# Performance work log

Measured on AMD Instinct MI355X. Metric: run time of the kernel, lower is better.

The kernel has to match this reference:

```python
import jax, jax.numpy as jnp
import numpy as np

C = 384; H = 32; W = 32; HEADS = 12; HD = C // HEADS; MLP = 1536
KOFF = 5; OFF_RANGE = 2.0


def layer_norm(x, g, b, eps=1e-5):
    mu = jnp.mean(x, axis=-1, keepdims=True)
    var = jnp.mean(jnp.square(x - mu), axis=-1, keepdims=True)
    return (x - mu) * jax.lax.rsqrt(var + eps) * g + b


def depthwise_conv(x, k):
    # x: (B,H,W,C), k: (kh,kw,1,C), SAME padding, groups=C
    return jax.lax.conv_general_dilated(
        x, k, window_strides=(1, 1), padding='SAME',
        dimension_numbers=('NHWC', 'HWIO', 'NHWC'), feature_group_count=C)


def grid_sample_bilinear(img, pos):
    # img: (B,H,W,C); pos: (B,H,W,2) normalized (y,x) in [-1,1], align_corners=True, border clamp
    B, Hh, Ww, Cc = img.shape
    py = (pos[..., 0] + 1.0) * 0.5 * (Hh - 1)
    px = (pos[..., 1] + 1.0) * 0.5 * (Ww - 1)
    y0 = jnp.floor(py); x0 = jnp.floor(px)
    wy = (py - y0)[..., None]; wx = (px - x0)[..., None]
    y0i = jnp.clip(y0.astype(jnp.int32), 0, Hh - 1)
    y1i = jnp.clip(y0i + 1, 0, Hh - 1)
    x0i = jnp.clip(x0.astype(jnp.int32), 0, Ww - 1)
    x1i = jnp.clip(x0i + 1, 0, Ww - 1)
    b = jnp.arange(B)[:, None, None]
    g = lambda yi, xi: img[b, yi, xi]
    return (g(y0i, x0i) * (1 - wy) * (1 - wx) + g(y0i, x1i) * (1 - wy) * wx
            + g(y1i, x0i) * wy * (1 - wx) + g(y1i, x1i) * wy * wx)


def setup_inputs() -> dict:
    key = jax.random.key(0)
    ks = jax.random.split(key, 16)
    n = jax.random.normal
    s = 0.02
    inp = {
        'x': n(ks[0], (16, H * W, C), jnp.float32),
        'ln1_g': jnp.ones((C,), jnp.float32), 'ln1_b': jnp.zeros((C,), jnp.float32),
        'Wq': n(ks[1], (C, C), jnp.float32) * s, 'bq': jnp.zeros((C,), jnp.float32),
        'off_k': n(ks[2], (KOFF, KOFF, 1, C), jnp.float32) * s,
        'off_kb': jnp.zeros((C,), jnp.float32),
        'offln_g': jnp.ones((C,), jnp.float32), 'offln_b': jnp.zeros((C,), jnp.float32),
        'Woff': n(ks[3], (2, C), jnp.float32) * s, 'boff': jnp.zeros((2,), jnp.float32),
        'Wk': n(ks[4], (C, C), jnp.float32) * s, 'bk': jnp.zeros((C,), jnp.float32),
        'Wv': n(ks[5], (C, C), jnp.float32) * s, 'bv': jnp.zeros((C,), jnp.float32),
        'Wo': n(ks[6], (C, C), jnp.float32) * s, 'bo': jnp.zeros((C,), jnp.float32),
        'ln2_g': jnp.ones((C,), jnp.float32), 'ln2_b': jnp.zeros((C,), jnp.float32),
        'W1': n(ks[7], (MLP, C), jnp.float32) * s, 'b1': jnp.zeros((MLP,), jnp.float32),
        'W2': n(ks[8], (C, MLP), jnp.float32) * s, 'b2': jnp.zeros((C,), jnp.float32),
    }
    return inp


def _block(x, ln1_g, ln1_b, Wq, bq, off_k, off_kb, offln_g, offln_b, Woff, boff,
           Wk, bk, Wv, bv, Wo, bo, ln2_g, ln2_b, W1, b1, W2, b2):
    B, N, _ = x.shape
    # --- deformable attention branch ---
    xn = layer_norm(x, ln1_g, ln1_b)
    xi = xn.reshape(B, H, W, C)
    q = xi @ Wq.T + bq                                  # (B,H,W,C)
    # offset network: depthwise conv -> LN -> GELU -> 1x1 conv to 2
    off = depthwise_conv(q, off_k) + off_kb
    off = jax.nn.gelu(layer_norm(off, offln_g, offln_b))
    off = off @ Woff.T + boff                           # (B,H,W,2)
    off_range = jnp.array([OFF_RANGE * 2.0 / H, OFF_RANGE * 2.0 / W], jnp.float32)
    off = jnp.tanh(off) * off_range                     # normalized coord units
    ry = (jnp.arange(H, dtype=jnp.float32) + 0.5) / H * 2.0 - 1.0
    rx = (jnp.arange(W, dtype=jnp.float32) + 0.5) / W * 2.0 - 1.0
    ref = jnp.stack(jnp.meshgrid(ry, rx, indexing='ij'), axis=-1)  # (H,W,2)
    pos = ref[None] + off                               # (B,H,W,2)
    xs = grid_sample_bilinear(xi, pos).reshape(B, N, C)  # sampled keys/values source
    k = xs @ Wk.T + bk
    v = xs @ Wv.T + bv
    qh = q.reshape(B, N, HEADS, HD).transpose(0, 2, 1, 3)
    kh = k.reshape(B, N, HEADS, HD).transpose(0, 2, 1, 3)
    vh = v.reshape(B, N, HEADS, HD).transpose(0, 2, 1, 3)
    attn = jax.nn.softmax(jnp.einsum('bhqd,bhkd->bhqk', qh, kh) * (HD ** -0.5), axis=-1)
    o = jnp.einsum('bhqk,bhkd->bhqd', attn, vh).transpose(0, 2, 1, 3).reshape(B, N, C)
    x = x + (o @ Wo.T + bo)
    # --- MLP branch ---
    y = layer_norm(x, ln2_g, ln2_b)
    y = jax.nn.gelu(y @ W1.T + b1) @ W2.T + b2
    return x + y


def reference(x, ln1_g, ln1_b, Wq, bq, off_k, off_kb, offln_g, offln_b, Woff, boff,
              Wk, bk, Wv, bv, Wo, bo, ln2_g, ln2_b, W1, b1, W2, b2):
    return _block(x, ln1_g, ln1_b, Wq, bq, off_k, off_kb, offln_g, offln_b, Woff, boff,
                  Wk, bk, Wv, bv, Wo, bo, ln2_g, ln2_b, W1, b1, W2, b2)
```

## Files before the change

### kernel.cpp

```cpp
#include <hip/hip_runtime.h>
#include <math.h>

#define DI __device__ __forceinline__

typedef __attribute__((ext_vector_type(8))) short bf16x8;
typedef __attribute__((ext_vector_type(4))) float f32x4;

static constexpr int CC = 384;
static constexpr float QSCALE = 0.17677669529663687f * 1.4426950408889634f;
static constexpr float INVQS  = 1.0f / QSCALE;

DI unsigned short f2bf(float f){
  unsigned u = __float_as_uint(f);
  u += 0x7FFFu + ((u >> 16) & 1u);
  return (unsigned short)(u >> 16);
}
DI float bf2f(unsigned short u){ return __uint_as_float((unsigned)u << 16); }
DI float lo16(unsigned u){ return __uint_as_float(u << 16); }
DI float hi16(unsigned u){ return __uint_as_float(u & 0xFFFF0000u); }
DI float fexp2(float x){ return __builtin_amdgcn_exp2f(x); }
DI float frcp(float x){ return __builtin_amdgcn_rcpf(x); }
DI float tanh_fast(float z){ return 1.f - 2.f*frcp(fexp2(2.8853900817779268f*z) + 1.f); }
DI float gelu_fast(float v){
  float u = v*v;
  float z = 0.7978845608028654f * fmaf(0.044715f*u, v, v);
  return v - v*frcp(fexp2(2.8853900817779268f*z) + 1.f);
}
DI f32x4 mfma16(bf16x8 a, bf16x8 b, f32x4 c){
  return __builtin_amdgcn_mfma_f32_16x16x32_bf16(a, b, c, 0, 0, 0);
}
DI void gload16(const unsigned short* g, unsigned short* l){
  __builtin_amdgcn_global_load_lds(
      (const __attribute__((address_space(1))) unsigned int*)(const void*)g,
      (__attribute__((address_space(3))) unsigned int*)(void*)l, 16, 0, 0);
}
DI unsigned packbf(float pa, float pb){
  return __builtin_amdgcn_perm(__float_as_uint(pb), __float_as_uint(pa), 0x07060302u);
}

__global__ __launch_bounds__(256) void k_cvt_all(
    const float* __restrict__ wq, const float* __restrict__ wk,
    const float* __restrict__ wv, const float* __restrict__ wo,
    const float* __restrict__ w1, const float* __restrict__ w2,
    const float* __restrict__ ofk,
    unsigned short* __restrict__ dst)
{
  int i4 = (blockIdx.x*256 + threadIdx.x)*4;
  if (i4 >= 1779072) return;
  const float* src; int off;
  if (i4 < 147456){ src = wq; off = i4; }
  else if (i4 < 294912){ src = wk; off = i4 - 147456; }
  else if (i4 < 442368){ src = wv; off = i4 - 294912; }
  else if (i4 < 589824){ src = wo; off = i4 - 442368; }
  else if (i4 < 1179648){ src = w1; off = i4 - 589824; }
  else if (i4 < 1769472){ src = w2; off = i4 - 1179648; }
  else { src = ofk; off = i4 - 1769472; }
  float4 v = *(const float4*)(src + off);
  uint2 o;
  o.x = ((unsigned)f2bf(v.y) << 16) | f2bf(v.x);
  o.y = ((unsigned)f2bf(v.w) << 16) | f2bf(v.z);
  *(uint2*)(dst + i4) = o;
}

template<int BIN>
__global__ __launch_bounds__(256) void k_ln(const float* __restrict__ xf,
    const unsigned short* __restrict__ xb,
    const float* __restrict__ g, const float* __restrict__ b,
    unsigned short* __restrict__ outb)
{
  int row = blockIdx.x*4 + (threadIdx.x >> 6);
  int l = threadIdx.x & 63;
  float v[6]; int ch[6];
  if constexpr (BIN){
    int cA = 4*l, cB = 256 + 2*l;
    ch[0]=cA; ch[1]=cA+1; ch[2]=cA+2; ch[3]=cA+3; ch[4]=cB; ch[5]=cB+1;
    const unsigned short* xp = xb + (size_t)row * CC;
    uint2 u2 = *(const uint2*)(xp + cA);
    unsigned u1 = *(const unsigned*)(xp + cB);
    v[0]=lo16(u2.x); v[1]=hi16(u2.x); v[2]=lo16(u2.y); v[3]=hi16(u2.y);
    v[4]=lo16(u1);   v[5]=hi16(u1);
  } else {
    const float* xp = xf + (size_t)row * CC;
#pragma unroll
    for (int p = 0; p < 6; p++){ ch[p] = l + 64*p; v[p] = xp[ch[p]]; }
  }
  float s = 0.f, s2 = 0.f;
#pragma unroll
  for (int p = 0; p < 6; p++){ s += v[p]; s2 += v[p]*v[p]; }
#pragma unroll
  for (int m = 32; m; m >>= 1){ s += __shfl_xor(s, m); s2 += __shfl_xor(s2, m); }
  float mu = s * (1.f/CC);
  float var = s2 * (1.f/CC) - mu*mu;
  float rs = rsqrtf(var + 1e-5f);
  float o[6];
#pragma unroll
  for (int p = 0; p < 6; p++) o[p] = (v[p] - mu) * rs * g[ch[p]] + b[ch[p]];
  unsigned short* op = outb + (size_t)row*CC;
  if constexpr (BIN){
    uint2 st;
    st.x = ((unsigned)f2bf(o[1]) << 16) | f2bf(o[0]);
    st.y = ((unsigned)f2bf(o[3]) << 16) | f2bf(o[2]);
    *(uint2*)(op + ch[0]) = st;
    *(unsigned*)(op + ch[4]) = ((unsigned)f2bf(o[5]) << 16) | f2bf(o[4]);
  } else {
#pragma unroll
    for (int p = 0; p < 6; p++) op[ch[p]] = f2bf(o[p]);
  }
}

template<int EPI>
__global__ __launch_bounds__(256) void k_gemm64(
    const unsigned short* __restrict__ A, const unsigned short* __restrict__ W,
    const float* __restrict__ bias, const float* __restrict__ bias2,
    const float* __restrict__ res, const unsigned short* __restrict__ resb,
    float* __restrict__ outf, unsigned short* __restrict__ outb,
    unsigned short* __restrict__ outb2, int ntn, int N, int K)
{
  __shared__ unsigned short As[2][2048];
  __shared__ unsigned short Bs[2][4096];
  int bid = blockIdx.x;
  int cpx = gridDim.x >> 3;
  int id = (bid & 7)*cpx + (bid >> 3);
  int bn = (id % ntn) * 128;
  int bm = (id / ntn) * 64;
  int t = threadIdx.x;
  int w = t >> 6, l = t & 63;
  int g = l >> 4, ln = l & 15;
  int wm = w >> 1, wn = w & 1;
  f32x4 acc[2][4];
#pragma unroll
  for (int i = 0; i < 2; i++)
#pragma unroll
    for (int j = 0; j < 4; j++) acc[i][j] = (f32x4){0.f,0.f,0.f,0.f};
  int srow = t >> 2, slot = t & 3;
  int srowB = srow + 64;
  int cb0 = (slot ^ (srow  & 3) ^ ((srow  >> 2) & 3)) * 8;
  int cb1 = (slot ^ (srowB & 3) ^ ((srowB >> 2) & 3)) * 8;
  const unsigned short* Ap  = A + (size_t)(bm + srow)*K + cb0;
  const unsigned short* Wp0 = W + (size_t)(bn + srow)*K + cb0;
  const unsigned short* Wp1 = W + (size_t)(bn + srowB)*K + cb1;
  int NT = K >> 5;
  int wl = w*512;
  gload16(Ap,  &As[0][wl]);
  gload16(Wp0, &Bs[0][wl]);
  gload16(Wp1, &Bs[0][wl + 2048]);
  __syncthreads();
  for (int kt = 0; kt < NT; kt++){
    int cur = kt & 1;
    if (kt + 1 < NT){
      int k0 = (kt + 1) << 5;
      gload16(Ap  + k0, &As[cur ^ 1][wl]);
      gload16(Wp0 + k0, &Bs[cur ^ 1][wl]);
      gload16(Wp1 + k0, &Bs[cur ^ 1][wl + 2048]);
    }
    bf16x8 af[2], bf[4];
#pragma unroll
    for (int mi = 0; mi < 2; mi++){
      int row = wm*32 + mi*16 + ln;
      int sl = g ^ (row & 3) ^ ((row >> 2) & 3);
      af[mi] = *(const bf16x8*)((const char*)As[cur] + row*64 + sl*16);
    }
#pragma unroll
    for (int ni = 0; ni < 4; ni++){
      int row = wn*64 + ni*16 + ln;
      int sl = g ^ (row & 3) ^ ((row >> 2) & 3);
      bf[ni] = *(const bf16x8*)((const char*)Bs[cur] + row*64 + sl*16);
    }
#pragma unroll
    for (int mi = 0; mi < 2; mi++)
#pragma unroll
      for (int ni = 0; ni < 4; ni++)
        acc[mi][ni] = mfma16(af[mi], bf[ni], acc[mi][ni]);
    if (kt + 1 < NT) __syncthreads();
  }
#pragma unroll
  for (int mi = 0; mi < 2; mi++)
#pragma unroll
  for (int ni = 0; ni < 4; ni++){
    int col = bn + wn*64 + ni*16 + ln;
    float bv;
    if constexpr (EPI == 6) bv = col < 384 ? bias[col] : bias2[col - 384];
    else bv = bias[col];
#pragma unroll
    for (int i = 0; i < 4; i++){
      int row = bm + wm*32 + mi*16 + g*4 + i;
      float v = acc[mi][ni][i] + bv;
      if constexpr (EPI == 2){ v += res[(size_t)row*N + col]; outb[(size_t)row*N + col] = f2bf(v); }
      if constexpr (EPI == 7){ v += bf2f(resb[(size_t)row*N + col]); outf[(size_t)row*N + col] = v; }
      if constexpr (EPI == 3) v = gelu_fast(v);
      if constexpr (EPI == 0) outf[(size_t)row*N + col] = v;
      if constexpr (EPI == 1 || EPI == 3) outb[(size_t)row*N + col] = f2bf(v);
      if constexpr (EPI == 5) outb[(size_t)row*N + col] = f2bf(v * QSCALE);
      if constexpr (EPI == 6){
        if (col < 384){
          outb[(size_t)row*384 + col] = f2bf(v);
        } else {
          int c = col - 384;
          int bb = row >> 10, key = row & 1023, h = c >> 5, d = c & 31;
          int k6 = key & 63;
          int phys = (key & ~63) | (k6 & 0x23) | ((k6 & 0xC) << 1) | ((k6 & 0x10) >> 2);
          outb2[(size_t)(((bb*12 + h) << 5) + d)*1024 + phys] = f2bf(v);
        }
      }
    }
  }
}

__global__ __launch_bounds__(256) void k_mlp1(
    const unsigned short* __restrict__ A, const unsigned short* __restrict__ W,
    const float* __restrict__ bias, unsigned short* __restrict__ outb)
{
  __shared__ unsigned short As[2][4096];
  __shared__ unsigned short Bs[2][4096];
  int bid = blockIdx.x;
  int cpx = gridDim.x >> 3;
  int id = (bid & 7)*cpx + (bid >> 3);
  int bn = (id % 12) * 128;
  int bm = (id / 12) * 128;
  int t = threadIdx.x;
  int w = t >> 6, l = t & 63;
  int g = l >> 4, ln = l & 15;
  int wm = w >> 1, wn = w & 1;
  f32x4 acc[4][4];
#pragma unroll
  for (int i = 0; i < 4; i++)
#pragma unroll
    for (int j = 0; j < 4; j++) acc[i][j] = (f32x4){0.f,0.f,0.f,0.f};
  int srow0 = t >> 2, slot = t & 3;
  int srow1 = srow0 + 64;
  int cb0 = (slot ^ (srow0 & 3) ^ ((srow0 >> 2) & 3)) * 8;
  int cb1 = (slot ^ (srow1 & 3) ^ ((srow1 >> 2) & 3)) * 8;
  const unsigned short* Ap0 = A + (size_t)(bm + srow0)*384 + cb0;
  const unsigned short* Ap1 = A + (size_t)(bm + srow1)*384 + cb1;
  const unsigned short* Wp0 = W + (size_t)(bn + srow0)*384 + cb0;
  const unsigned short* Wp1 = W + (size_t)(bn + srow1)*384 + cb1;
  int wl = w*512;
  gload16(Ap0, &As[0][wl]);
  gload16(Ap1, &As[0][wl + 2048]);
  gload16(Wp0, &Bs[0][wl]);
  gload16(Wp1, &Bs[0][wl + 2048]);
  __syncthreads();
  for (int kt = 0; kt < 12; kt++){
    int cur = kt & 1;
    if (kt < 11){
      int k0 = (kt + 1) << 5;
      gload16(Ap0 + k0, &As[cur ^ 1][wl]);
      gload16(Ap1 + k0, &As[cur ^ 1][wl + 2048]);
      gload16(Wp0 + k0, &Bs[cur ^ 1][wl]);
      gload16(Wp1 + k0, &Bs[cur ^ 1][wl + 2048]);
    }
    bf16x8 af[4], bf[4];
#pragma unroll
    for (int mi = 0; mi < 4; mi++){
      int row = wm*64 + mi*16 + ln;
      int sl = g ^ (row & 3) ^ ((row >> 2) & 3);
      af[mi] = *(const bf16x8*)((const char*)As[cur] + row*64 + sl*16);
    }
#pragma unroll
    for (int ni = 0; ni < 4; ni++){
      int row = wn*64 + ni*16 + ln;
      int sl = g ^ (row & 3) ^ ((row >> 2) & 3);
      bf[ni] = *(const bf16x8*)((const char*)Bs[cur] + row*64 + sl*16);
    }
#pragma unroll
    for (int mi = 0; mi < 4; mi++)
#pragma unroll
      for (int ni = 0; ni < 4; ni++)
        acc[mi][ni] = mfma16(af[mi], bf[ni], acc[mi][ni]);
    if (kt < 11) __syncthreads();
  }
#pragma unroll
  for (int mi = 0; mi < 4; mi++)
#pragma unroll
  for (int ni = 0; ni < 4; ni++){
    int col = bn + wn*64 + ni*16 + ln;
    float bv = bias[col];
#pragma unroll
    for (int i = 0; i < 4; i++){
      int row = bm + wm*64 + mi*16 + g*4 + i;
      float v = gelu_fast(acc[mi][ni][i] + bv);
      outb[(size_t)row*1536 + col] = f2bf(v);
    }
  }
}

__global__ __launch_bounds__(64) void k_offset_sample(
    const unsigned short* __restrict__ qs, const unsigned short* __restrict__ xnb,
    const unsigned short* __restrict__ okb,
    const float* __restrict__ offkb,
    const float* __restrict__ offg, const float* __restrict__ offb,
    const float* __restrict__ Woff, const float* __restrict__ boff,
    unsigned short* __restrict__ xsb)
{
  int blk = blockIdx.x;
  int pix = (blk & 7)*2048 + (blk >> 3);
  int b = pix >> 10, n = pix & 1023;
  int y = n >> 5, x = n & 31;
  int t = threadIdx.x;
  int c8 = (t < 48 ? t : 47) * 8;
  float act = t < 48 ? 1.f : 0.f;
  const unsigned short* qb = qs + (size_t)b*1024*CC;
  int ry[5], rx[5]; unsigned my[5], mx[5];
#pragma unroll
  for (int k = 0; k < 5; k++){
    int yy = y + k - 2, xx = x + k - 2;
    my[k] = (yy >= 0 && yy < 32) ? 0xFFFFFFFFu : 0u;
    mx[k] = (xx >= 0 && xx < 32) ? 0xFFFFFFFFu : 0u;
    int yc = yy < 0 ? 0 : (yy > 31 ? 31 : yy);
    int xc = xx < 0 ? 0 : (xx > 31 ? 31 : xx);
    ry[k] = yc*32*CC; rx[k] = xc*CC;
  }
  float a[8];
#pragma unroll
  for (int j = 0; j < 8; j++) a[j] = 0.f;
#pragma unroll
  for (int ky = 0; ky < 5; ky++)
#pragma unroll
  for (int kx = 0; kx < 5; kx++){
    int tap = ky*5 + kx;
    unsigned m = my[ky] & mx[kx];
    uint4 q4 = *(const uint4*)(qb + ry[ky] + rx[kx] + c8);
    uint4 w4 = *(const uint4*)(okb + tap*CC + c8);
    q4.x &= m; q4.y &= m; q4.z &= m; q4.w &= m;
    a[0] = fmaf(lo16(q4.x), lo16(w4.x), a[0]);
    a[1] = fmaf(hi16(q4.x), hi16(w4.x), a[1]);
    a[2] = fmaf(lo16(q4.y), lo16(w4.y), a[2]);
    a[3] = fmaf(hi16(q4.y), hi16(w4.y), a[3]);
    a[4] = fmaf(lo16(q4.z), lo16(w4.z), a[4]);
    a[5] = fmaf(hi16(q4.z), hi16(w4.z), a[5]);
    a[6] = fmaf(lo16(q4.w), lo16(w4.w), a[6]);
    a[7] = fmaf(hi16(q4.w), hi16(w4.w), a[7]);
  }
  float4 kbA = *(const float4*)(offkb + c8);
  float4 kbB = *(const float4*)(offkb + c8 + 4);
  float c[8];
  c[0] = act * fmaf(a[0], INVQS, kbA.x);
  c[1] = act * fmaf(a[1], INVQS, kbA.y);
  c[2] = act * fmaf(a[2], INVQS, kbA.z);
  c[3] = act * fmaf(a[3], INVQS, kbA.w);
  c[4] = act * fmaf(a[4], INVQS, kbB.x);
  c[5] = act * fmaf(a[5], INVQS, kbB.y);
  c[6] = act * fmaf(a[6], INVQS, kbB.z);
  c[7] = act * fmaf(a[7], INVQS, kbB.w);
  float s = 0.f, s2 = 0.f;
#pragma unroll
  for (int j = 0; j < 8; j++){ s += c[j]; s2 += c[j]*c[j]; }
#pragma unroll
  for (int m2 = 32; m2; m2 >>= 1){ s += __shfl_xor(s, m2); s2 += __shfl_xor(s2, m2); }
  float mu = s * (1.f/CC);
  float var = s2 * (1.f/CC) - mu*mu;
  float rs = rsqrtf(var + 1e-5f);
  float4 gA = *(const float4*)(offg + c8); float4 gB = *(const float4*)(offg + c8 + 4);
  float4 oA = *(const float4*)(offb + c8); float4 oB = *(const float4*)(offb + c8 + 4);
  float4 wA = *(const float4*)(Woff + c8); float4 wB = *(const float4*)(Woff + c8 + 4);
  float4 wC = *(const float4*)(Woff + CC + c8); float4 wD = *(const float4*)(Woff + CC + c8 + 4);
  float gg[8] = {gA.x,gA.y,gA.z,gA.w,gB.x,gB.y,gB.z,gB.w};
  float bb[8] = {oA.x,oA.y,oA.z,oA.w,oB.x,oB.y,oB.z,oB.w};
  float w0[8] = {wA.x,wA.y,wA.z,wA.w,wB.x,wB.y,wB.z,wB.w};
  float w1[8] = {wC.x,wC.y,wC.z,wC.w,wD.x,wD.y,wD.z,wD.w};
  float p0 = 0.f, p1 = 0.f;
#pragma unroll
  for (int j = 0; j < 8; j++){
    float v = gelu_fast((c[j] - mu)*rs*gg[j] + bb[j]) * act;
    p0 = fmaf(v, w0[j], p0);
    p1 = fmaf(v, w1[j], p1);
  }
#pragma unroll
  for (int m2 = 32; m2; m2 >>= 1){ p0 += __shfl_xor(p0, m2); p1 += __shfl_xor(p1, m2); }
  float offy = tanh_fast(p0 + boff[0]) * 0.125f;
  float offx = tanh_fast(p1 + boff[1]) * 0.125f;
  float py = ((y + 0.5f)/16.f - 1.f + offy + 1.f) * 0.5f * 31.f;
  float px = ((x + 0.5f)/16.f - 1.f + offx + 1.f) * 0.5f * 31.f;
  float y0f = floorf(py), x0f = floorf(px);
  float wy = py - y0f, wx = px - x0f;
  int y0 = (int)y0f, x0 = (int)x0f;
  y0 = y0 < 0 ? 0 : (y0 > 31 ? 31 : y0);
  x0 = x0 < 0 ? 0 : (x0 > 31 ? 31 : x0);
  int y1 = y0 + 1 > 31 ? 31 : y0 + 1;
  int x1 = x0 + 1 > 31 ? 31 : x0 + 1;
  const unsigned short* s00 = xnb + (size_t)(b*1024 + y0*32 + x0)*CC + c8;
  const unsigned short* s01 = xnb + (size_t)(b*1024 + y0*32 + x1)*CC + c8;
  const unsigned short* s10 = xnb + (size_t)(b*1024 + y1*32 + x0)*CC + c8;
  const unsigned short* s11 = xnb + (size_t)(b*1024 + y1*32 + x1)*CC + c8;
  float w00 = (1.f-wy)*(1.f-wx), w01 = (1.f-wy)*wx, w10 = wy*(1.f-wx), w11 = wy*wx;
  uint4 A0 = *(const uint4*)s00;
  uint4 A1 = *(const uint4*)s01;
  uint4 A2 = *(const uint4*)s10;
  uint4 A3 = *(const uint4*)s11;
  if (t < 48){
    float r[8];
    r[0] = w00*lo16(A0.x) + w01*lo16(A1.x) + w10*lo16(A2.x) + w11*lo16(A3.x);
    r[1] = w00*hi16(A0.x) + w01*hi16(A1.x) + w10*hi16(A2.x) + w11*hi16(A3.x);
    r[2] = w00*lo16(A0.y) + w01*lo16(A1.y) + w10*lo16(A2.y) + w11*lo16(A3.y);
    r[3] = w00*hi16(A0.y) + w01*hi16(A1.y) + w10*hi16(A2.y) + w11*hi16(A3.y);
    r[4] = w00*lo16(A0.z) + w01*lo16(A1.z) + w10*lo16(A2.z) + w11*lo16(A3.z);
    r[5] = w00*hi16(A0.z) + w01*hi16(A1.z) + w10*hi16(A2.z) + w11*hi16(A3.z);
    r[6] = w00*lo16(A0.w) + w01*lo16(A1.w) + w10*lo16(A2.w) + w11*lo16(A3.w);
    r[7] = w00*hi16(A0.w) + w01*hi16(A1.w) + w10*hi16(A2.w) + w11*hi16(A3.w);
    uint4 st;
    st.x = ((unsigned)f2bf(r[1]) << 16) | f2bf(r[0]);
    st.y = ((unsigned)f2bf(r[3]) << 16) | f2bf(r[2]);
    st.z = ((unsigned)f2bf(r[5]) << 16) | f2bf(r[4]);
    st.w = ((unsigned)f2bf(r[7]) << 16) | f2bf(r[6]);
    *(uint4*)(xsb + (size_t)(b*1024 + n)*CC + c8) = st;
  }
}

__global__ __launch_bounds__(256) void k_attn(
    const unsigned short* __restrict__ qs, const unsigned short* __restrict__ kb,
    const unsigned short* __restrict__ vt, unsigned short* __restrict__ ob)
{
  __shared__ unsigned short Ks[2][64][40];
  __shared__ unsigned short Vs[2][32][72];
  int blk = blockIdx.x;
  int sw = (blk & 7)*192 + (blk >> 3);
  int qt = sw & 7, h = (sw >> 3) % 12, b = sw / 96;
  int t = threadIdx.x;
  int w = t >> 6, l = t & 63;
  int g = l >> 4, ln = l & 15;
  int q0 = qt*128 + w*32;
  bf16x8 qa[2];
#pragma unroll
  for (int mi = 0; mi < 2; mi++)
    qa[mi] = *(const bf16x8*)&qs[(size_t)(b*1024 + q0 + mi*16 + ln)*CC + h*32 + g*8];
  bf16x8 vones;
#pragma unroll
  for (int j = 0; j < 8; j++) vones[j] = (short)0x3F80;
  f32x4 z = {0.f,0.f,0.f,0.f};
  f32x4 oacc[2][2]; oacc[0][0]=z; oacc[0][1]=z; oacc[1][0]=z; oacc[1][1]=z;
  f32x4 lacc[2]; lacc[0]=z; lacc[1]=z;
  int krow = t >> 2, kc = (t & 3)*8;
  int vdim = t >> 3, vc = (t & 7)*8;
  const unsigned short* kptr = kb + (size_t)(b*1024 + krow)*CC + h*32 + kc;
  const unsigned short* vptr = vt + (size_t)((b*12 + h)*32 + vdim)*1024 + vc;
  {
    uint4 kr = *(const uint4*)kptr;
    uint4 vr = *(const uint4*)vptr;
    *(uint4*)&Ks[0][krow][kc] = kr;
    *(uint4*)&Vs[0][vdim][vc] = vr;
  }
  __syncthreads();
  for (int kt = 0; kt < 16; kt++){
    int cur = kt & 1;
    uint4 kr2, vr2;
    if (kt < 15){
      int k0 = (kt + 1)*64;
      kr2 = *(const uint4*)(kptr + (size_t)k0*CC);
      vr2 = *(const uint4*)(vptr + k0);
    }
    bf16x8 kf[4];
#pragma unroll
    for (int nt = 0; nt < 4; nt++) kf[nt] = *(const bf16x8*)&Ks[cur][nt*16 + ln][g*8];
    f32x4 st[2][4];
    __builtin_amdgcn_s_setprio(1);
#pragma unroll
    for (int mi = 0; mi < 2; mi++)
#pragma unroll
      for (int nt = 0; nt < 4; nt++) st[mi][nt] = mfma16(kf[nt], qa[mi], z);
    __builtin_amdgcn_s_setprio(0);
    bf16x8 pa[2][2];
#pragma unroll
    for (int mi = 0; mi < 2; mi++){
#pragma unroll
      for (int k2 = 0; k2 < 2; k2++){
        float e0 = fexp2(st[mi][2*k2][0]),   e1 = fexp2(st[mi][2*k2][1]);
        float e2 = fexp2(st[mi][2*k2][2]),   e3 = fexp2(st[mi][2*k2][3]);
        float f0 = fexp2(st[mi][2*k2+1][0]), f1 = fexp2(st[mi][2*k2+1][1]);
        float f2 = fexp2(st[mi][2*k2+1][2]), f3 = fexp2(st[mi][2*k2+1][3]);
        uint4 pw;
        pw.x = packbf(e0, e1);
        pw.y = packbf(e2, e3);
        pw.z = packbf(f0, f1);
        pw.w = packbf(f2, f3);
        pa[mi][k2] = *(bf16x8*)&pw;
      }
    }
    __builtin_amdgcn_s_setprio(1);
#pragma unroll
    for (int k2 = 0; k2 < 2; k2++){
      bf16x8 va[2];
#pragma unroll
      for (int d2 = 0; d2 < 2; d2++) va[d2] = *(const bf16x8*)&Vs[cur][d2*16 + ln][k2*32 + g*8];
#pragma unroll
      for (int mi = 0; mi < 2; mi++){
#pragma unroll
        for (int d2 = 0; d2 < 2; d2++) oacc[mi][d2] = mfma16(pa[mi][k2], va[d2], oacc[mi][d2]);
        lacc[mi] = mfma16(pa[mi][k2], vones, lacc[mi]);
      }
    }
    __builtin_amdgcn_s_setprio(0);
    if (kt < 15){
      *(uint4*)&Ks[cur ^ 1][krow][kc] = kr2;
      *(uint4*)&Vs[cur ^ 1][vdim][vc] = vr2;
      __syncthreads();
    }
  }
  float rinv[2][4];
#pragma unroll
  for (int mi = 0; mi < 2; mi++)
#pragma unroll
    for (int i = 0; i < 4; i++) rinv[mi][i] = frcp(lacc[mi][i]);
#pragma unroll
  for (int mi = 0; mi < 2; mi++)
#pragma unroll
  for (int d2 = 0; d2 < 2; d2++)
#pragma unroll
  for (int i = 0; i < 4; i++){
    float v = oacc[mi][d2][i] * rinv[mi][i];
    int row = q0 + mi*16 + g*4 + i;
    ob[(size_t)(b*1024 + row)*CC + h*32 + d2*16 + ln] = f2bf(v);
  }
}

extern "C" void kernel_launch(void* const* d_in, const int* in_sizes, int n_in,
                              void* d_out, int out_size, void* d_ws, size_t ws_size,
                              hipStream_t stream)
{
  (void)in_sizes; (void)n_in; (void)out_size; (void)ws_size;
  const float* x     = (const float*)d_in[0];
  const float* ln1g  = (const float*)d_in[1];
  const float* ln1b  = (const float*)d_in[2];
  const float* Wq    = (const float*)d_in[3];
  const float* bq    = (const float*)d_in[4];
  const float* offk  = (const float*)d_in[5];
  const float* offkb = (const float*)d_in[6];
  const float* offg  = (const float*)d_in[7];
  const float* offb  = (const float*)d_in[8];
  const float* Woff  = (const float*)d_in[9];
  const float* boff  = (const float*)d_in[10];
  const float* Wk    = (const float*)d_in[11];
  const float* bk    = (const float*)d_in[12];
  const float* Wv    = (const float*)d_in[13];
  const float* bv    = (const float*)d_in[14];
  const float* Wo    = (const float*)d_in[15];
  const float* bo    = (const float*)d_in[16];
  const float* ln2g  = (const float*)d_in[17];
  const float* ln2b  = (const float*)d_in[18];
  const float* W1    = (const float*)d_in[19];
  const float* b1    = (const float*)d_in[20];
  const float* W2    = (const float*)d_in[21];
  const float* b2    = (const float*)d_in[22];

  char* ws = (char*)d_ws;
  unsigned short* X2B = (unsigned short*)ws;
  unsigned short* XSB = (unsigned short*)(ws + 25165824);
  unsigned short* KB  = (unsigned short*)(ws + 37748736);
  unsigned short* VT  = (unsigned short*)(ws + 50331648);
  unsigned short* OB  = (unsigned short*)(ws + 62914560);
  unsigned short* XNB = (unsigned short*)(ws + 75497472);
  unsigned short* QSB = (unsigned short*)(ws + 88080384);
  unsigned short* YB  = QSB;
  unsigned short* HB  = (unsigned short*)(ws + 25165824);
  unsigned short* WQB = (unsigned short*)(ws + 100663296);
  unsigned short* WKB = WQB + 147456;
  unsigned short* WOB = WKB + 294912;
  unsigned short* W1B = WOB + 147456;
  unsigned short* W2B = W1B + 589824;
  unsigned short* OKB = W2B + 589824;

  k_cvt_all<<<1738, 256, 0, stream>>>(Wq, Wk, Wv, Wo, W1, W2, offk, WQB);
  k_ln<0><<<4096, 256, 0, stream>>>(x, nullptr, ln1g, ln1b, XNB);
  k_gemm64<5><<<768, 256, 0, stream>>>(XNB, WQB, bq, nullptr, nullptr, nullptr, nullptr, QSB, nullptr, 3, 384, 384);
  k_offset_sample<<<16384, 64, 0, stream>>>(QSB, XNB, OKB, offkb, offg, offb, Woff, boff, XSB);
  k_gemm64<6><<<1536, 256, 0, stream>>>(XSB, WKB, bk, bv, nullptr, nullptr, nullptr, KB, VT, 6, 768, 384);
  k_attn<<<1536, 256, 0, stream>>>(QSB, KB, VT, OB);
  k_gemm64<2><<<768, 256, 0, stream>>>(OB, WOB, bo, nullptr, x, nullptr, nullptr, X2B, nullptr, 3, 384, 384);
  k_ln<1><<<4096, 256, 0, stream>>>(nullptr, X2B, ln2g, ln2b, YB);
  k_mlp1<<<1536, 256, 0, stream>>>(YB, W1B, b1, HB);
  k_gemm64<7><<<768, 256, 0, stream>>>(HB, W2B, b2, nullptr, nullptr, X2B, (float*)d_out, nullptr, nullptr, 3, 384, 1536);
}
```

Before: 235.3 us.

## Enlarge attention query tile and add dedicated swizzled MLP2 GEMM kernel

The attention kernel now gives each wave 64 query rows instead of 32, halving the grid. This reuses each staged K/V tile across twice as many queries, and score, exp and PV MFMAs are interleaved per key sub-block to keep fewer score registers live. A new k_mlp2 kernel replaces the generic gemm64 for the down projection, using 64x128 tiles with XOR-swizzled LDS, async global-to-LDS loads and a fused bias plus bf16 residual epilogue. The trade-off is higher register pressure and fewer blocks in attention.

```diff
diff --git a/kernel.cpp b/kernel.cpp
--- a/kernel.cpp
+++ b/kernel.cpp
@@ -280,6 +280,92 @@
       int row = bm + wm*64 + mi*16 + g*4 + i;
       float v = gelu_fast(acc[mi][ni][i] + bv);
       outb[(size_t)row*1536 + col] = f2bf(v);
+    }
+  }
+}
+
+__global__ __launch_bounds__(256) void k_mlp2(
+    const unsigned short* __restrict__ A, const unsigned short* __restrict__ W,
+    const float* __restrict__ bias, const unsigned short* __restrict__ resb,
+    float* __restrict__ outf)
+{
+  __shared__ unsigned short As[2][4096];
+  __shared__ unsigned short Bs[2][8192];
+  int bid = blockIdx.x;
+  int cpx = gridDim.x >> 3;
+  int id = (bid & 7)*cpx + (bid >> 3);
+  int bn = (id % 3) * 128;
+  int bm = (id / 3) * 64;
+  int t = threadIdx.x;
+  int w = t >> 6, l = t & 63;
+  int g = l >> 4, ln = l & 15;
+  int wm = w >> 1, wn = w & 1;
+  f32x4 acc[2][4];
+#pragma unroll
+  for (int i = 0; i < 2; i++)
+#pragma unroll
+    for (int j = 0; j < 4; j++) acc[i][j] = (f32x4){0.f,0.f,0.f,0.f};
+  int srcoff = ((t & 7) ^ ((t >> 3) & 7)) * 8;
+  int srowA = t >> 3;
+  const unsigned short* Ap0 = A + (size_t)(bm + srowA)*1536 + srcoff;
+  const unsigned short* Ap1 = A + (size_t)(bm + 32 + srowA)*1536 + srcoff;
+  const unsigned short* Wp0 = W + (size_t)(bn + srowA)*1536 + srcoff;
+  const unsigned short* Wp1 = W + (size_t)(bn + 32 + srowA)*1536 + srcoff;
+  const unsigned short* Wp2 = W + (size_t)(bn + 64 + srowA)*1536 + srcoff;
+  const unsigned short* Wp3 = W + (size_t)(bn + 96 + srowA)*1536 + srcoff;
+  int wl = w*512;
+  gload16(Ap0, &As[0][wl]);
+  gload16(Ap1, &As[0][wl + 2048]);
+  gload16(Wp0, &Bs[0][wl]);
+  gload16(Wp1, &Bs[0][wl + 2048]);
+  gload16(Wp2, &Bs[0][wl + 4096]);
+  gload16(Wp3, &Bs[0][wl + 6144]);
+  __syncthreads();
+  for (int kt = 0; kt < 24; kt++){
+    int cur = kt & 1;
+    if (kt < 23){
+      int k0 = (kt + 1) << 6;
+      gload16(Ap0 + k0, &As[cur ^ 1][wl]);
+      gload16(Ap1 + k0, &As[cur ^ 1][wl + 2048]);
+      gload16(Wp0 + k0, &Bs[cur ^ 1][wl]);
+      gload16(Wp1 + k0, &Bs[cur ^ 1][wl + 2048]);
+      gload16(Wp2 + k0, &Bs[cur ^ 1][wl + 4096]);
+      gload16(Wp3 + k0, &Bs[cur ^ 1][wl + 6144]);
+    }
+#pragma unroll
+    for (int kk = 0; kk < 2; kk++){
+      bf16x8 af[2], bf[4];
+#pragma unroll
+      for (int mi = 0; mi < 2; mi++){
+        int row = wm*32 + mi*16 + ln;
+        int sl = (kk*4 + g) ^ (row & 7);
+        af[mi] = *(const bf16x8*)((const char*)As[cur] + row*128 + sl*16);
+      }
+#pragma unroll
+      for (int ni = 0; ni < 4; ni++){
+        int row = wn*64 + ni*16 + ln;
+        int sl = (kk*4 + g) ^ (row & 7);
+        bf[ni] = *(const bf16x8*)((const char*)Bs[cur] + row*128 + sl*16);
+      }
+#pragma unroll
+      for (int mi = 0; mi < 2; mi++)
+#pragma unroll
+        for (int ni = 0; ni < 4; ni++)
+          acc[mi][ni] = mfma16(af[mi], bf[ni], acc[mi][ni]);
+    }
+    if (kt < 23) __syncthreads();
+  }
+#pragma unroll
+  for (int mi = 0; mi < 2; mi++)
+#pragma unroll
+  for (int ni = 0; ni < 4; ni++){
+    int col = bn + wn*64 + ni*16 + ln;
+    float bv = bias[col];
+#pragma unroll
+    for (int i = 0; i < 4; i++){
+      int row = bm + wm*32 + mi*16 + g*4 + i;
+      float v = acc[mi][ni][i] + bv + bf2f(resb[(size_t)row*384 + col]);
+      outf[(size_t)row*384 + col] = v;
     }
   }
 }
@@ -413,22 +499,24 @@
   __shared__ unsigned short Ks[2][64][40];
   __shared__ unsigned short Vs[2][32][72];
   int blk = blockIdx.x;
-  int sw = (blk & 7)*192 + (blk >> 3);
-  int qt = sw & 7, h = (sw >> 3) % 12, b = sw / 96;
+  int sw = (blk & 7)*96 + (blk >> 3);
+  int qt = sw & 3, h = (sw >> 2) % 12, b = sw / 48;
   int t = threadIdx.x;
   int w = t >> 6, l = t & 63;
   int g = l >> 4, ln = l & 15;
-  int q0 = qt*128 + w*32;
-  bf16x8 qa[2];
-#pragma unroll
-  for (int mi = 0; mi < 2; mi++)
+  int q0 = qt*256 + w*64;
+  bf16x8 qa[4];
+#pragma unroll
+  for (int mi = 0; mi < 4; mi++)
     qa[mi] = *(const bf16x8*)&qs[(size_t)(b*1024 + q0 + mi*16 + ln)*CC + h*32 + g*8];
   bf16x8 vones;
 #pragma unroll
   for (int j = 0; j < 8; j++) vones[j] = (short)0x3F80;
   f32x4 z = {0.f,0.f,0.f,0.f};
-  f32x4 oacc[2][2]; oacc[0][0]=z; oacc[0][1]=z; oacc[1][0]=z; oacc[1][1]=z;
-  f32x4 lacc[2]; lacc[0]=z; lacc[1]=z;
+  f32x4 oacc[4][2];
+#pragma unroll
+  for (int mi = 0; mi < 4; mi++){ oacc[mi][0]=z; oacc[mi][1]=z; }
+  f32x4 lacc[4]; lacc[0]=z; lacc[1]=z; lacc[2]=z; lacc[3]=z;
   int krow = t >> 2, kc = (t & 3)*8;
   int vdim = t >> 3, vc = (t & 7)*8;
   const unsigned short* kptr = kb + (size_t)(b*1024 + krow)*CC + h*32 + kc;
@@ -448,60 +536,46 @@
       kr2 = *(const uint4*)(kptr + (size_t)k0*CC);
       vr2 = *(const uint4*)(vptr + k0);
     }
-    bf16x8 kf[4];
-#pragma unroll
-    for (int nt = 0; nt < 4; nt++) kf[nt] = *(const bf16x8*)&Ks[cur][nt*16 + ln][g*8];
-    f32x4 st[2][4];
-    __builtin_amdgcn_s_setprio(1);
-#pragma unroll
-    for (int mi = 0; mi < 2; mi++)
-#pragma unroll
-      for (int nt = 0; nt < 4; nt++) st[mi][nt] = mfma16(kf[nt], qa[mi], z);
-    __builtin_amdgcn_s_setprio(0);
-    bf16x8 pa[2][2];
-#pragma unroll
-    for (int mi = 0; mi < 2; mi++){
-#pragma unroll
-      for (int k2 = 0; k2 < 2; k2++){
-        float e0 = fexp2(st[mi][2*k2][0]),   e1 = fexp2(st[mi][2*k2][1]);
-        float e2 = fexp2(st[mi][2*k2][2]),   e3 = fexp2(st[mi][2*k2][3]);
-        float f0 = fexp2(st[mi][2*k2+1][0]), f1 = fexp2(st[mi][2*k2+1][1]);
-        float f2 = fexp2(st[mi][2*k2+1][2]), f3 = fexp2(st[mi][2*k2+1][3]);
+#pragma unroll
+    for (int k2 = 0; k2 < 2; k2++){
+      bf16x8 kf0 = *(const bf16x8*)&Ks[cur][(2*k2)*16 + ln][g*8];
+      bf16x8 kf1 = *(const bf16x8*)&Ks[cur][(2*k2+1)*16 + ln][g*8];
+      bf16x8 va0 = *(const bf16x8*)&Vs[cur][ln][k2*32 + g*8];
+      bf16x8 va1 = *(const bf16x8*)&Vs[cur][16 + ln][k2*32 + g*8];
+      __builtin_amdgcn_s_setprio(1);
+#pragma unroll
+      for (int mi = 0; mi < 4; mi++){
+        f32x4 s0 = mfma16(kf0, qa[mi], z);
+        f32x4 s1 = mfma16(kf1, qa[mi], z);
+        float e0 = fexp2(s0[0]), e1 = fexp2(s0[1]);
+        float e2 = fexp2(s0[2]), e3 = fexp2(s0[3]);
+        float f0 = fexp2(s1[0]), f1 = fexp2(s1[1]);
+        float f2 = fexp2(s1[2]), f3 = fexp2(s1[3]);
         uint4 pw;
         pw.x = packbf(e0, e1);
         pw.y = packbf(e2, e3);
         pw.z = packbf(f0, f1);
         pw.w = packbf(f2, f3);
-        pa[mi][k2] = *(bf16x8*)&pw;
+        bf16x8 pa = *(bf16x8*)&pw;
+        oacc[mi][0] = mfma16(pa, va0, oacc[mi][0]);
+        oacc[mi][1] = mfma16(pa, va1, oacc[mi][1]);
+        lacc[mi] = mfma16(pa, vones, lacc[mi]);
       }
-    }
-    __builtin_amdgcn_s_setprio(1);
-#pragma unroll
-    for (int k2 = 0; k2 < 2; k2++){
-      bf16x8 va[2];
-#pragma unroll
-      for (int d2 = 0; d2 < 2; d2++) va[d2] = *(const bf16x8*)&Vs[cur][d2*16 + ln][k2*32 + g*8];
-#pragma unroll
-      for (int mi = 0; mi < 2; mi++){
-#pragma unroll
-        for (int d2 = 0; d2 < 2; d2++) oacc[mi][d2] = mfma16(pa[mi][k2], va[d2], oacc[mi][d2]);
-        lacc[mi] = mfma16(pa[mi][k2], vones, lacc[mi]);
-      }
-    }
-    __builtin_amdgcn_s_setprio(0);
+      __builtin_amdgcn_s_setprio(0);
+    }
     if (kt < 15){
       *(uint4*)&Ks[cur ^ 1][krow][kc] = kr2;
       *(uint4*)&Vs[cur ^ 1][vdim][vc] = vr2;
       __syncthreads();
     }
   }
-  float rinv[2][4];
-#pragma unroll
-  for (int mi = 0; mi < 2; mi++)
+  float rinv[4][4];
+#pragma unroll
+  for (int mi = 0; mi < 4; mi++)
 #pragma unroll
     for (int i = 0; i < 4; i++) rinv[mi][i] = frcp(lacc[mi][i]);
 #pragma unroll
-  for (int mi = 0; mi < 2; mi++)
+  for (int mi = 0; mi < 4; mi++)
 #pragma unroll
   for (int d2 = 0; d2 < 2; d2++)
 #pragma unroll
@@ -563,9 +637,9 @@
   k_gemm64<5><<<768, 256, 0, stream>>>(XNB, WQB, bq, nullptr, nullptr, nullptr, nullptr, QSB, nullptr, 3, 384, 384);
   k_offset_sample<<<16384, 64, 0, stream>>>(QSB, XNB, OKB, offkb, offg, offb, Woff, boff, XSB);
   k_gemm64<6><<<1536, 256, 0, stream>>>(XSB, WKB, bk, bv, nullptr, nullptr, nullptr, KB, VT, 6, 768, 384);
-  k_attn<<<1536, 256, 0, stream>>>(QSB, KB, VT, OB);
+  k_attn<<<768, 256, 0, stream>>>(QSB, KB, VT, OB);
   k_gemm64<2><<<768, 256, 0, stream>>>(OB, WOB, bo, nullptr, x, nullptr, nullptr, X2B, nullptr, 3, 384, 384);
   k_ln<1><<<4096, 256, 0, stream>>>(nullptr, X2B, ln2g, ln2b, YB);
   k_mlp1<<<1536, 256, 0, stream>>>(YB, W1B, b1, HB);
-  k_gemm64<7><<<768, 256, 0, stream>>>(HB, W2B, b2, nullptr, nullptr, X2B, (float*)d_out, nullptr, nullptr, 3, 384, 1536);
-}
+  k_mlp2<<<768, 256, 0, stream>>>(HB, W2B, b2, X2B, (float*)d_out);
+}
```

After: 223.0 us. 1.06x faster.
